# Optimization experiments

Measured on AMD Instinct MI355X. Metric: run time of the kernel, lower is better.

Reference implementation:

```python
import jax, jax.numpy as jnp
import numpy as np

B, S, H, NH = 16, 384, 1024, 16
HD = H // NH  # head_dim = 64

def setup_inputs() -> dict:
    key = jax.random.key(0)
    k1, k2, k3 = jax.random.split(key, 3)
    activation = jax.random.normal(k1, (B, S, H), dtype=jnp.float32)
    attention_mask = jnp.zeros((B, 1, 1, S), dtype=jnp.float32)  # additive mask
    qkv_weight = jax.random.normal(k2, (H, 3 * H), dtype=jnp.float32) * 0.02
    qkv_bias = jax.random.normal(k3, (3 * H,), dtype=jnp.float32) * 0.02
    return {"activation": activation, "attention_mask": attention_mask,
            "qkv_weight": qkv_weight, "qkv_bias": qkv_bias}

def reference(activation, attention_mask, qkv_weight, qkv_bias):
    # op1: fused QKV projection
    qkv = activation @ qkv_weight + qkv_bias            # [B,S,3H]
    q, k, v = jnp.split(qkv, 3, axis=-1)                # each [B,S,H]
    # op2-6: split heads -> [B,NH,S,HD]
    def heads(x):
        return x.reshape(B, S, NH, HD).transpose(0, 2, 1, 3)
    q, k, v = heads(q), heads(k), heads(v)
    # op7: QK^T
    scores = jnp.einsum('bhqd,bhkd->bhqk', q, k)        # [B,NH,S,S]
    # op8: scale + mask + softmax (scale applied to scores, then additive mask)
    scale = 1.0 / np.sqrt(HD).astype(np.float32)
    probs = jax.nn.softmax(scores * scale + attention_mask, axis=-1)
    # op9: weighted V
    out = jnp.einsum('bhqk,bhkd->bhqd', probs, v)       # [B,NH,S,HD]
    # op10: concat heads
    return out.transpose(0, 2, 1, 3).reshape(B, S, H)
```

## Files before the change

### kernel.cpp

```cpp
#include <hip/hip_runtime.h>
#include <hip/hip_bf16.h>

#define BB 16
#define SS 384
#define HH 1024
#define NH 16
#define HD 64
#define MM (BB*SS)
#define KK HH
#define N3 (3*HH)

typedef float f32x4 __attribute__((ext_vector_type(4)));
typedef __bf16 bf16x8 __attribute__((ext_vector_type(8)));
typedef unsigned short us8 __attribute__((ext_vector_type(8)));
typedef unsigned short us4 __attribute__((ext_vector_type(4)));

__device__ __forceinline__ void gload_lds16(const void* g, void* l) {
    __builtin_amdgcn_global_load_lds(
        (const __attribute__((address_space(1))) void*)g,
        (__attribute__((address_space(3))) void*)l, 16, 0, 0);
}

__device__ __forceinline__ unsigned short f2b(float f) {
    __bf16 h = (__bf16)f;
    return __builtin_bit_cast(unsigned short, h);
}

__global__ __launch_bounds__(256) void cvt_x(const float4* __restrict__ in,
                                             us4* __restrict__ out, int n4) {
    int i = blockIdx.x * 256 + threadIdx.x;
    if (i < n4) {
        float4 v = in[i];
        us4 o;
        o.x = f2b(v.x); o.y = f2b(v.y); o.z = f2b(v.z); o.w = f2b(v.w);
        out[i] = o;
    }
}

__global__ __launch_bounds__(256) void cvt_w(const float* __restrict__ Wf,
                                             __bf16* __restrict__ WT) {
    __shared__ float tile[32][33];
    const int n0 = blockIdx.x * 32, k0 = blockIdx.y * 32;
    const int t = threadIdx.x;
    const int tj = t & 31, ti = t >> 5;
#pragma unroll
    for (int p = 0; p < 4; ++p) {
        int i = p * 8 + ti;
        tile[i][tj] = Wf[(size_t)(k0 + i) * N3 + n0 + tj];
    }
    __syncthreads();
#pragma unroll
    for (int p = 0; p < 4; ++p) {
        int jj = p * 8 + ti;
        WT[(size_t)(n0 + jj) * KK + k0 + tj] = (__bf16)tile[tj][jj];
    }
}

__global__ __launch_bounds__(256) void qkv_gemm(const __bf16* __restrict__ Xb,
                                                const __bf16* __restrict__ WT,
                                                const float* __restrict__ bias,
                                                __bf16* __restrict__ QKb,
                                                __bf16* __restrict__ VTg) {
    __shared__ __bf16 As[128 * 32];
    __shared__ __bf16 Bs[128 * 32];
    const int t = threadIdx.x;
    const int w = t >> 6, lane = t & 63;
    const int wr = w >> 1, wc = w & 1;
    const int l15 = lane & 15, lg = lane >> 4;
    const int m0 = blockIdx.y * 128, n0 = blockIdx.x * 128;

    f32x4 acc[4][4] = {};

    for (int k0 = 0; k0 < KK; k0 += 32) {
#pragma unroll
        for (int i = 0; i < 2; ++i) {
            int slab = w * 2 + i;
            int row = slab * 16 + (lane >> 2);
            int ck = lane & 3;
            gload_lds16(Xb + (size_t)(m0 + row) * KK + k0 + ck * 8, &As[slab * 512]);
            gload_lds16(WT + (size_t)(n0 + row) * KK + k0 + ck * 8, &Bs[slab * 512]);
        }
        __syncthreads();

        bf16x8 a[4];
#pragma unroll
        for (int i = 0; i < 4; ++i) {
            int row = wr * 64 + i * 16 + l15;
            a[i] = *(const bf16x8*)&As[row * 32 + lg * 8];
        }
#pragma unroll
        for (int j = 0; j < 4; ++j) {
            int row = wc * 64 + j * 16 + l15;
            bf16x8 bv = *(const bf16x8*)&Bs[row * 32 + lg * 8];
#pragma unroll
            for (int i = 0; i < 4; ++i)
                acc[i][j] = __builtin_amdgcn_mfma_f32_16x16x32_bf16(a[i], bv, acc[i][j], 0, 0, 0);
        }
        __syncthreads();
    }

#pragma unroll
    for (int j = 0; j < 4; ++j) {
        int c = n0 + wc * 64 + j * 16 + l15;
        float bv = bias[c];
#pragma unroll
        for (int i = 0; i < 4; ++i) {
#pragma unroll
            for (int r = 0; r < 4; ++r) {
                int rr = m0 + wr * 64 + i * 16 + lg * 4 + r;
                float v = acc[i][j][r] + bv;
                if (c < 2048) {
                    QKb[(size_t)rr * 2048 + c] = (__bf16)v;
                } else {
                    int d = c & 63;
                    int hh = (c - 2048) >> 6;
                    int bb = rr / SS;
                    int s = rr - bb * SS;
                    VTg[((size_t)(bb * NH + hh) * HD + d) * SS + s] = (__bf16)v;
                }
            }
        }
    }
}

#define SMEMSZ 49152

__global__ __launch_bounds__(256, 3) void attn(const __bf16* __restrict__ QKb,
                                               const __bf16* __restrict__ VTg,
                                               const float* __restrict__ maskg,
                                               float* __restrict__ out) {
    extern __shared__ char smem[];
    const int bid = blockIdx.x;
    const int xcd = bid & 7, idx = bid >> 3;
    const int head = xcd * 32 + idx / 6;
    const int qt = idx - (idx / 6) * 6;
    const int b = head >> 4, h = head & 15;
    const int q0 = qt * 64;
    const int t = threadIdx.x;
    const int w = t >> 6, lane = t & 63;
    const int l15 = lane & 15, lg = lane >> 4;

    const size_t qrow = (size_t)(b * SS + q0 + w * 16 + l15) * 2048 + h * 64;
    bf16x8 aq[2];
#pragma unroll
    for (int st = 0; st < 2; ++st)
        aq[st] = *(const bf16x8*)&QKb[qrow + st * 32 + lg * 8];

    f32x4 acc[24];
#pragma unroll
    for (int f = 0; f < 24; ++f) acc[f] = f32x4{0.f, 0.f, 0.f, 0.f};
#pragma unroll
    for (int f = 0; f < 24; ++f) {
        const size_t krow = (size_t)(b * SS + f * 16 + l15) * 2048 + 1024 + h * 64;
#pragma unroll
        for (int st = 0; st < 2; ++st) {
            bf16x8 kb = *(const bf16x8*)&QKb[krow + st * 32 + lg * 8];
            acc[f] = __builtin_amdgcn_mfma_f32_16x16x32_bf16(aq[st], kb, acc[f], 0, 0, 0);
        }
    }

    const float* mrow = maskg + b * SS;
    float mx[4] = {-1e30f, -1e30f, -1e30f, -1e30f};
#pragma unroll
    for (int f = 0; f < 24; ++f) {
        float mk = mrow[f * 16 + l15];
#pragma unroll
        for (int r = 0; r < 4; ++r) {
            float v = acc[f][r] * 0.125f + mk;
            acc[f][r] = v;
            mx[r] = fmaxf(mx[r], v);
        }
    }
#pragma unroll
    for (int off = 8; off >= 1; off >>= 1)
#pragma unroll
        for (int r = 0; r < 4; ++r) mx[r] = fmaxf(mx[r], __shfl_xor(mx[r], off, 64));
    float sm[4] = {0.f, 0.f, 0.f, 0.f};
#pragma unroll
    for (int f = 0; f < 24; ++f)
#pragma unroll
        for (int r = 0; r < 4; ++r) {
            float p = __expf(acc[f][r] - mx[r]);
            acc[f][r] = p;
            sm[r] += p;
        }
#pragma unroll
    for (int off = 8; off >= 1; off >>= 1)
#pragma unroll
        for (int r = 0; r < 4; ++r) sm[r] += __shfl_xor(sm[r], off, 64);
    float inv[4];
#pragma unroll
    for (int r = 0; r < 4; ++r) inv[r] = 1.f / sm[r];

#pragma unroll
    for (int f = 0; f < 24; ++f)
#pragma unroll
        for (int r = 0; r < 4; ++r) {
            int row = w * 16 + lg * 4 + r;
            int col = f * 16 + l15;
            int byte = (row * 768 + col * 2) ^ ((row & 7) << 4);
            *(__bf16*)(smem + byte) = (__bf16)acc[f][r];
        }
    __syncthreads();

    f32x4 o[4] = {};
    const int prow = w * 16 + l15;
#pragma unroll
    for (int st = 0; st < 12; ++st) {
        bf16x8 pa = *(const bf16x8*)(smem +
                     ((prow * 768 + st * 64 + lg * 16) ^ ((prow & 7) << 4)));
#pragma unroll
        for (int j = 0; j < 4; ++j) {
            bf16x8 vb = *(const bf16x8*)&VTg[((size_t)head * HD + j * 16 + l15) * SS
                                             + st * 32 + lg * 8];
            o[j] = __builtin_amdgcn_mfma_f32_16x16x32_bf16(pa, vb, o[j], 0, 0, 0);
        }
    }

#pragma unroll
    for (int j = 0; j < 4; ++j)
#pragma unroll
        for (int r = 0; r < 4; ++r) {
            int qr = q0 + w * 16 + lg * 4 + r;
            out[(size_t)(b * SS + qr) * HH + h * 64 + j * 16 + l15] =
                o[j][r] * inv[r];
        }
}

extern "C" void kernel_launch(void* const* d_in, const int* in_sizes, int n_in,
                              void* d_out, int out_size, void* d_ws, size_t ws_size,
                              hipStream_t stream) {
    const float* act  = (const float*)d_in[0];
    const float* mask = (const float*)d_in[1];
    const float* wq   = (const float*)d_in[2];
    const float* bias = (const float*)d_in[3];

    char* ws = (char*)d_ws;
    __bf16* Xb  = (__bf16*)(ws);
    __bf16* WT  = (__bf16*)(ws + 12582912);
    __bf16* QKb = (__bf16*)(ws + 18874368);
    __bf16* VTg = (__bf16*)(ws + 44040192);

    cvt_x<<<(MM * KK / 4 + 255) / 256, 256, 0, stream>>>((const float4*)act, (us4*)Xb, MM * KK / 4);
    cvt_w<<<dim3(N3 / 32, KK / 32), 256, 0, stream>>>(wq, WT);
    qkv_gemm<<<dim3(N3 / 128, MM / 128), 256, 0, stream>>>(Xb, WT, bias, QKb, VTg);

    (void)hipFuncSetAttribute((const void*)attn, hipFuncAttributeMaxDynamicSharedMemorySize, SMEMSZ);
    attn<<<BB * NH * 6, 256, SMEMSZ, stream>>>(QKb, VTg, mask, (float*)d_out);
}
```

Before: 165.4 us.

## Stage K and V per head in LDS and compute S^T to keep P in registers

```diff
diff --git a/kernel.cpp b/kernel.cpp
--- a/kernel.cpp
+++ b/kernel.cpp
@@ -14,6 +14,7 @@
 typedef __bf16 bf16x8 __attribute__((ext_vector_type(8)));
 typedef unsigned short us8 __attribute__((ext_vector_type(8)));
 typedef unsigned short us4 __attribute__((ext_vector_type(4)));
+typedef unsigned int u32x4 __attribute__((ext_vector_type(4)));
 
 __device__ __forceinline__ void gload_lds16(const void* g, void* l) {
     __builtin_amdgcn_global_load_lds(
@@ -123,108 +124,138 @@
     }
 }
 
-#define SMEMSZ 49152
-
-__global__ __launch_bounds__(256, 3) void attn(const __bf16* __restrict__ QKb,
-                                               const __bf16* __restrict__ VTg,
-                                               const float* __restrict__ maskg,
-                                               float* __restrict__ out) {
+#define AKLOFF 0
+#define AVTOFF 49152
+#define AMKOFF 98304
+#define ASMEM  99840
+
+__global__ __launch_bounds__(512) void attn(const __bf16* __restrict__ QKb,
+                                            const __bf16* __restrict__ VTg,
+                                            const float* __restrict__ maskg,
+                                            float* __restrict__ out) {
     extern __shared__ char smem[];
-    const int bid = blockIdx.x;
-    const int xcd = bid & 7, idx = bid >> 3;
-    const int head = xcd * 32 + idx / 6;
-    const int qt = idx - (idx / 6) * 6;
+    const int head = blockIdx.x;
     const int b = head >> 4, h = head & 15;
-    const int q0 = qt * 64;
     const int t = threadIdx.x;
-    const int w = t >> 6, lane = t & 63;
+    const int wv = t >> 6, lane = t & 63;
     const int l15 = lane & 15, lg = lane >> 4;
 
-    const size_t qrow = (size_t)(b * SS + q0 + w * 16 + l15) * 2048 + h * 64;
-    bf16x8 aq[2];
-#pragma unroll
-    for (int st = 0; st < 2; ++st)
-        aq[st] = *(const bf16x8*)&QKb[qrow + st * 32 + lg * 8];
-
-    f32x4 acc[24];
-#pragma unroll
-    for (int f = 0; f < 24; ++f) acc[f] = f32x4{0.f, 0.f, 0.f, 0.f};
-#pragma unroll
-    for (int f = 0; f < 24; ++f) {
-        const size_t krow = (size_t)(b * SS + f * 16 + l15) * 2048 + 1024 + h * 64;
-#pragma unroll
-        for (int st = 0; st < 2; ++st) {
-            bf16x8 kb = *(const bf16x8*)&QKb[krow + st * 32 + lg * 8];
-            acc[f] = __builtin_amdgcn_mfma_f32_16x16x32_bf16(aq[st], kb, acc[f], 0, 0, 0);
-        }
-    }
-
-    const float* mrow = maskg + b * SS;
-    float mx[4] = {-1e30f, -1e30f, -1e30f, -1e30f};
-#pragma unroll
-    for (int f = 0; f < 24; ++f) {
-        float mk = mrow[f * 16 + l15];
+    bf16x8 bq[3][2];
+#pragma unroll
+    for (int c = 0; c < 3; ++c) {
+        const size_t qr = (size_t)(b * SS + (wv + 8 * c) * 16 + l15) * 2048 + h * 64;
+#pragma unroll
+        for (int st = 0; st < 2; ++st)
+            bq[c][st] = *(const bf16x8*)&QKb[qr + st * 32 + lg * 8];
+    }
+
+    for (int it = 0; it < 6; ++it) {
+        int slot = it * 512 + t;
+        int row = slot >> 3, ck = slot & 7;
+        us8 v = *(const us8*)&QKb[(size_t)(b * SS + row) * 2048 + 1024 + h * 64 + ck * 8];
+        int byte = (row * 128 + ck * 16) ^ ((row & 7) << 4);
+        *(us8*)(smem + AKLOFF + byte) = v;
+    }
+    for (int it = 0; it < 6; ++it) {
+        int slot = it * 512 + t;
+        int d = slot / 48, ck = slot - d * 48;
+        us8 v = *(const us8*)&VTg[((size_t)head * HD + d) * SS + ck * 8];
+        int byte = (d * 768 + ck * 16) ^ ((d & 7) << 4);
+        *(us8*)(smem + AVTOFF + byte) = v;
+    }
+    if (t < SS) ((float*)(smem + AMKOFF))[t] = maskg[b * SS + t];
+    __syncthreads();
+
+    const int srcA = l15 + 32 * (lg & 1);
+    const int srcB = srcA + 16;
+    const float* mrow = (const float*)(smem + AMKOFF);
+
+#pragma unroll
+    for (int c = 0; c < 3; ++c) {
+        const int q0c = (wv + 8 * c) * 16;
+
+        f32x4 acc[24];
+#pragma unroll
+        for (int f = 0; f < 24; ++f) acc[f] = f32x4{0.f, 0.f, 0.f, 0.f};
+#pragma unroll
+        for (int f = 0; f < 24; ++f) {
+            int row = f * 16 + l15;
+#pragma unroll
+            for (int st = 0; st < 2; ++st) {
+                bf16x8 kb = *(const bf16x8*)(smem + AKLOFF +
+                             ((row * 128 + st * 64 + lg * 16) ^ ((row & 7) << 4)));
+                acc[f] = __builtin_amdgcn_mfma_f32_16x16x32_bf16(kb, bq[c][st], acc[f], 0, 0, 0);
+            }
+        }
+
+        float mx = -1e30f;
+#pragma unroll
+        for (int f = 0; f < 24; ++f) {
+            float4 mk = *(const float4*)(mrow + f * 16 + 4 * lg);
+            acc[f][0] = acc[f][0] * 0.125f + mk.x;
+            acc[f][1] = acc[f][1] * 0.125f + mk.y;
+            acc[f][2] = acc[f][2] * 0.125f + mk.z;
+            acc[f][3] = acc[f][3] * 0.125f + mk.w;
+            mx = fmaxf(mx, fmaxf(fmaxf(acc[f][0], acc[f][1]), fmaxf(acc[f][2], acc[f][3])));
+        }
+        mx = fmaxf(mx, __shfl_xor(mx, 16, 64));
+        mx = fmaxf(mx, __shfl_xor(mx, 32, 64));
+
+        float sm = 0.f;
+#pragma unroll
+        for (int f = 0; f < 24; ++f) {
+#pragma unroll
+            for (int r = 0; r < 4; ++r) {
+                float p = __expf(acc[f][r] - mx);
+                acc[f][r] = p;
+                sm += p;
+            }
+        }
+        sm += __shfl_xor(sm, 16, 64);
+        sm += __shfl_xor(sm, 32, 64);
+        const float inv = 1.f / sm;
+
+        unsigned pk0[24], pk1[24];
+#pragma unroll
+        for (int f = 0; f < 24; ++f) {
+            pk0[f] = (unsigned)f2b(acc[f][0]) | ((unsigned)f2b(acc[f][1]) << 16);
+            pk1[f] = (unsigned)f2b(acc[f][2]) | ((unsigned)f2b(acc[f][3]) << 16);
+        }
+
+        u32x4 paw[12];
+#pragma unroll
+        for (int f = 0; f < 24; ++f) {
+            unsigned a0 = __shfl(pk0[f], srcA, 64);
+            unsigned a1 = __shfl(pk1[f], srcA, 64);
+            unsigned b0 = __shfl(pk0[f], srcB, 64);
+            unsigned b1 = __shfl(pk1[f], srcB, 64);
+            if ((lg >> 1) == (f & 1))
+                paw[f >> 1] = u32x4{a0, a1, b0, b1};
+        }
+
+        f32x4 o[4] = {};
+#pragma unroll
+        for (int st = 0; st < 12; ++st) {
+            bf16x8 pa = __builtin_bit_cast(bf16x8, paw[st]);
+#pragma unroll
+            for (int j = 0; j < 4; ++j) {
+                int d = j * 16 + l15;
+                bf16x8 vb = *(const bf16x8*)(smem + AVTOFF +
+                             ((d * 768 + st * 64 + lg * 16) ^ ((d & 7) << 4)));
+                o[j] = __builtin_amdgcn_mfma_f32_16x16x32_bf16(pa, vb, o[j], 0, 0, 0);
+            }
+        }
+
 #pragma unroll
         for (int r = 0; r < 4; ++r) {
-            float v = acc[f][r] * 0.125f + mk;
-            acc[f][r] = v;
-            mx[r] = fmaxf(mx[r], v);
-        }
-    }
-#pragma unroll
-    for (int off = 8; off >= 1; off >>= 1)
-#pragma unroll
-        for (int r = 0; r < 4; ++r) mx[r] = fmaxf(mx[r], __shfl_xor(mx[r], off, 64));
-    float sm[4] = {0.f, 0.f, 0.f, 0.f};
-#pragma unroll
-    for (int f = 0; f < 24; ++f)
-#pragma unroll
-        for (int r = 0; r < 4; ++r) {
-            float p = __expf(acc[f][r] - mx[r]);
-            acc[f][r] = p;
-            sm[r] += p;
-        }
-#pragma unroll
-    for (int off = 8; off >= 1; off >>= 1)
-#pragma unroll
-        for (int r = 0; r < 4; ++r) sm[r] += __shfl_xor(sm[r], off, 64);
-    float inv[4];
-#pragma unroll
-    for (int r = 0; r < 4; ++r) inv[r] = 1.f / sm[r];
-
-#pragma unroll
-    for (int f = 0; f < 24; ++f)
-#pragma unroll
-        for (int r = 0; r < 4; ++r) {
-            int row = w * 16 + lg * 4 + r;
-            int col = f * 16 + l15;
-            int byte = (row * 768 + col * 2) ^ ((row & 7) << 4);
-            *(__bf16*)(smem + byte) = (__bf16)acc[f][r];
-        }
-    __syncthreads();
-
-    f32x4 o[4] = {};
-    const int prow = w * 16 + l15;
-#pragma unroll
-    for (int st = 0; st < 12; ++st) {
-        bf16x8 pa = *(const bf16x8*)(smem +
-                     ((prow * 768 + st * 64 + lg * 16) ^ ((prow & 7) << 4)));
-#pragma unroll
-        for (int j = 0; j < 4; ++j) {
-            bf16x8 vb = *(const bf16x8*)&VTg[((size_t)head * HD + j * 16 + l15) * SS
-                                             + st * 32 + lg * 8];
-            o[j] = __builtin_amdgcn_mfma_f32_16x16x32_bf16(pa, vb, o[j], 0, 0, 0);
-        }
-    }
-
-#pragma unroll
-    for (int j = 0; j < 4; ++j)
-#pragma unroll
-        for (int r = 0; r < 4; ++r) {
-            int qr = q0 + w * 16 + lg * 4 + r;
-            out[(size_t)(b * SS + qr) * HH + h * 64 + j * 16 + l15] =
-                o[j][r] * inv[r];
-        }
+            float invr = __shfl(inv, 4 * lg + r, 64);
+            int qr = q0c + 4 * lg + r;
+#pragma unroll
+            for (int j = 0; j < 4; ++j)
+                out[(size_t)(b * SS + qr) * HH + h * 64 + j * 16 + l15] =
+                    o[j][r] * invr;
+        }
+    }
 }
 
 extern "C" void kernel_launch(void* const* d_in, const int* in_sizes, int n_in,
@@ -245,6 +276,6 @@
     cvt_w<<<dim3(N3 / 32, KK / 32), 256, 0, stream>>>(wq, WT);
     qkv_gemm<<<dim3(N3 / 128, MM / 128), 256, 0, stream>>>(Xb, WT, bias, QKb, VTg);
 
-    (void)hipFuncSetAttribute((const void*)attn, hipFuncAttributeMaxDynamicSharedMemorySize, SMEMSZ);
-    attn<<<BB * NH * 6, 256, SMEMSZ, stream>>>(QKb, VTg, mask, (float*)d_out);
-}
+    (void)hipFuncSetAttribute((const void*)attn, hipFuncAttributeMaxDynamicSharedMemorySize, ASMEM);
+    attn<<<BB * NH, 512, ASMEM, stream>>>(QKb, VTg, mask, (float*)d_out);
+}
```

Measured after the change: 136.0 us. 1.22x faster.
